# Kernel optimization log

Measured on AMD Instinct MI355X. Metric: run time of the kernel, lower is better.

## Reference

```python
import jax, jax.numpy as jnp
import numpy as np

EPS = 1e-5

def rms_norm(x, scale, eps=EPS):
    rms = jax.lax.rsqrt(jnp.mean(x * x, axis=-1, keepdims=True) + eps)
    return scale * (x * rms)

def act_quant(x, min_scale=0.001, max_scale=1000.0):
    # int8 activation quantization (STE in torch; fwd math only here)
    max_val = jnp.max(jnp.abs(x), axis=-1, keepdims=True)
    s = jnp.clip(127.0 / (max_val + 1e-5), min_scale, max_scale)
    return jnp.clip(jnp.round(s * x), -128.0, 127.0) / s

def weight_quant(w, num_bits=8):
    qmax = 2.0 ** (num_bits - 1) - 1.0
    scale = qmax / (jnp.max(jnp.abs(w)) + 1e-5)
    return jnp.round(jnp.clip(w * scale, -(qmax + 1.0), qmax)) / scale

def ternarize(w):
    sf = jnp.clip(1.0 / (jnp.mean(jnp.abs(w)) + 1e-5), 1e-4, 1e4)
    return jnp.sign(w * sf)

def setup_inputs() -> dict:
    key = jax.random.key(0)
    ks = jax.random.split(key, 5)
    B, S, E, H = 8, 512, 2048, 2048
    x = jax.random.normal(ks[0], (B, S, E), dtype=jnp.float32)
    # ternary {-1,0,1} init as in ternary_initialize
    def tern_init(k, shape):
        r = jax.random.uniform(k, shape, dtype=jnp.float32)
        return jnp.where(r < 1.0 / 3.0, -1.0, jnp.where(r > 2.0 / 3.0, 1.0, 0.0))
    return {
        "x": x,
        "rms_scale": jnp.ones((H,), jnp.float32),
        "W_f": tern_init(ks[1], (E, H)),
        "W_c": tern_init(ks[2], (E, H)),
        "W_g": tern_init(ks[3], (H, E)),
        "b_f": jnp.ones((H,), jnp.float32),
        "b_c": jnp.zeros((H,), jnp.float32),
        "b_g": jnp.zeros((H,), jnp.float32),
    }

def reference(x, rms_scale, W_f, W_c, W_g, b_f, b_c, b_g):
    B, S, E = x.shape
    H = W_f.shape[1]
    # quantize + ternarize weights once (identical every timestep)
    Wt_f = ternarize(weight_quant(W_f))
    Wt_c = ternarize(weight_quant(W_c))
    Wt_g = ternarize(weight_quant(W_g))  # (H, E) but E == H

    def step(h, x_t):
        xq = act_quant(rms_norm(x_t, rms_scale))
        # matmul-free linear: x @ (pos_mask - neg_mask) == x @ sign(W)
        f_t = jax.nn.sigmoid(xq @ Wt_f + b_f)
        c_t = jax.nn.silu(xq @ Wt_c + b_c)
        g_t = jax.nn.sigmoid(xq @ Wt_g + b_g)
        h_new = f_t * h + (1.0 - f_t) * c_t
        o_t = g_t * h_new
        # layer-level copy gate: sigmoid(W_g @ x_t^T)^T = sigmoid(x_t @ W_g^T), raw weights
        cg = jax.nn.sigmoid(x_t @ W_g.T)
        h_out = cg * x_t + (1.0 - cg) * h_new
        return h_out, o_t

    h0 = jnp.zeros((B, H), x.dtype)
    _, outs = jax.lax.scan(step, h0, jnp.swapaxes(x, 0, 1))  # scan over S
    return jnp.swapaxes(outs, 0, 1)  # (B, S, H)
```

## Files before the change

### kernel.cpp

```cpp
#include <hip/hip_runtime.h>
#include <hip/hip_bf16.h>
#include <cstdint>
#include <cstddef>

#define RTOT 4096
#define DIM  2048
#define NCAT 6144
#define NCHUNK 32
#define TCHUNK 16
#define NT 32

typedef __attribute__((ext_vector_type(4))) int int4v;

__device__ __forceinline__ float fast_sigmoid(float z) {
    return __builtin_amdgcn_rcpf(1.0f + __expf(-z));
}
__device__ __forceinline__ unsigned short f2h(float f) {
    union { _Float16 h; unsigned short u; } v; v.h = (_Float16)f; return v.u;
}
__device__ __forceinline__ float h2f(unsigned short u) {
    union { _Float16 h; unsigned short u; } v; v.u = u; return (float)v.h;
}

#define GLDS(gp, lp) __builtin_amdgcn_global_load_lds( \
    (__attribute__((address_space(1))) const void*)(gp), \
    (__attribute__((address_space(3))) void*)(lp), 16, 0, 0)

__device__ __forceinline__ int4v frag_ld(const signed char* p, int R, int lq) {
    return *(const int4v*)(p + R * 64 + ((lq ^ ((R >> 1) & 3)) * 16));
}

__global__ __launch_bounds__(256) void prep_all(
    const float* __restrict__ x, const float* __restrict__ scale,
    const float* __restrict__ Wf, const float* __restrict__ Wc,
    const float* __restrict__ Wg,
    signed char* __restrict__ WcatT, signed char* __restrict__ Wgb,
    signed char* __restrict__ Xq, signed char* __restrict__ Q1,
    signed char* __restrict__ Q2, float* __restrict__ s_arr,
    float* __restrict__ s1_arr)
{
    __shared__ __align__(16) char smem[4224];
    int bid = blockIdx.x;
    int tid = threadIdx.x;
    if (bid < 3072) {
        signed char (*tile)[65] = (signed char(*)[65])smem;
        int j0 = (bid % 96) * 64;
        int k0 = (bid / 96) * 64;
        const float* W = (j0 < 2048) ? Wf : (j0 < 4096) ? Wc : Wg;
        int jb = j0 & 2047;
        int c  = tid & 63;
        int rr = tid >> 6;
#pragma unroll
        for (int p = 0; p < 16; ++p) {
            int kl = p * 4 + rr;
            tile[kl][c] = (signed char)(int)W[(size_t)(k0 + kl) * DIM + jb + c];
        }
        __syncthreads();
#pragma unroll
        for (int p = 0; p < 16; ++p) {
            int jl = p * 4 + rr;
            WcatT[(size_t)(j0 + jl) * DIM + k0 + c] = tile[c][jl];
        }
    } else if (bid < 4096) {
        int idx = (bid - 3072) * 4096 + tid * 16;
#pragma unroll
        for (int p = 0; p < 4; ++p) {
            float4 v = *(const float4*)(Wg + idx + p * 4);
            char4 o;
            o.x = (signed char)(int)v.x; o.y = (signed char)(int)v.y;
            o.z = (signed char)(int)v.z; o.w = (signed char)(int)v.w;
            *(char4*)(Wgb + idx + p * 4) = o;
        }
    } else {
        int row = (bid - 4096) * 4 + (tid >> 6);
        int lane = tid & 63;
        const float* xr = x + (size_t)row * DIM;
        float xs[32], ys[32];
        float sum = 0.f, mx2 = 0.f;
#pragma unroll
        for (int sw = 0; sw < 4; ++sw) {
            int base = sw * 512 + lane * 8;
            float4 a0 = *(const float4*)(xr + base);
            float4 a1 = *(const float4*)(xr + base + 4);
            xs[sw * 8 + 0] = a0.x; xs[sw * 8 + 1] = a0.y;
            xs[sw * 8 + 2] = a0.z; xs[sw * 8 + 3] = a0.w;
            xs[sw * 8 + 4] = a1.x; xs[sw * 8 + 5] = a1.y;
            xs[sw * 8 + 6] = a1.z; xs[sw * 8 + 7] = a1.w;
        }
#pragma unroll
        for (int i = 0; i < 32; ++i) {
            sum += xs[i] * xs[i];
            mx2 = fmaxf(mx2, fabsf(xs[i]));
        }
#pragma unroll
        for (int off = 1; off < 64; off <<= 1) {
            sum += __shfl_xor(sum, off);
            mx2 = fmaxf(mx2, __shfl_xor(mx2, off));
        }
        float rms = 1.0f / sqrtf(sum * (1.0f / 2048.0f) + 1e-5f);
        float mx = 0.f;
#pragma unroll
        for (int sw = 0; sw < 4; ++sw) {
            int base = sw * 512 + lane * 8;
            float4 c0 = *(const float4*)(scale + base);
            float4 c1 = *(const float4*)(scale + base + 4);
            float scv[8] = {c0.x, c0.y, c0.z, c0.w, c1.x, c1.y, c1.z, c1.w};
#pragma unroll
            for (int i = 0; i < 8; ++i) {
                float yv = (xs[sw * 8 + i] * rms) * scv[i];
                ys[sw * 8 + i] = yv;
                mx = fmaxf(mx, fabsf(yv));
            }
        }
#pragma unroll
        for (int off = 1; off < 64; off <<= 1) mx = fmaxf(mx, __shfl_xor(mx, off));
        float s = 127.0f / (mx + 1e-5f);
        s = fminf(fmaxf(s, 0.001f), 1000.0f);
        float s1 = 127.0f / (mx2 + 1e-5f);
        float inv_s1 = 1.0f / s1;
        if (lane == 0) { s_arr[row] = s; s1_arr[row] = s1; }
#pragma unroll
        for (int sw = 0; sw < 4; ++sw) {
            signed char q8[8], q1b[8], q2b[8];
#pragma unroll
            for (int i = 0; i < 8; ++i) {
                float xv = xs[sw * 8 + i];
                float q = fminf(fmaxf(rintf(s * ys[sw * 8 + i]), -128.f), 127.f);
                q8[i] = (signed char)(int)q;
                float qq1 = fminf(fmaxf(rintf(s1 * xv), -128.f), 127.f);
                q1b[i] = (signed char)(int)qq1;
                float r = xv - qq1 * inv_s1;
                float qq2 = fminf(fmaxf(rintf(s1 * 256.f * r), -128.f), 127.f);
                q2b[i] = (signed char)(int)qq2;
            }
            size_t o = (size_t)row * DIM + sw * 512 + lane * 8;
            *(int2*)(Xq + o) = *(int2*)q8;
            *(int2*)(Q1 + o) = *(int2*)q1b;
            *(int2*)(Q2 + o) = *(int2*)q2b;
        }
    }
}

__global__ __launch_bounds__(512, 2) void gemm_all(
    const signed char* __restrict__ Xq, const signed char* __restrict__ WcatT,
    const signed char* __restrict__ Q1, const signed char* __restrict__ Q2,
    const signed char* __restrict__ Wgb,
    const float* __restrict__ s_arr, const float* __restrict__ s1_arr,
    const float* __restrict__ b_f, const float* __restrict__ b_c,
    const float* __restrict__ b_g,
    unsigned short* __restrict__ FCG,
    unsigned short* __restrict__ U,
    unsigned short* __restrict__ V)
{
    extern __shared__ __align__(16) signed char lds[];
    int bid = blockIdx.x;
    int grp = bid / 5, r5 = bid % 5;
    int tid = threadIdx.x;
    int lane = tid & 63, wv = tid >> 6;
    int lr = lane & 15, lq = lane >> 4;
    int srow = wv * 16 + (lane >> 2);
    int ssw  = ((lane & 3) ^ ((srow >> 1) & 3)) * 16;
    const size_t ustep = (size_t)128 * DIM;

    if (r5 < 3) {
        int fb = grp * 3 + r5;
        int m0 = (fb & 15) * 256;
        int n0 = (fb >> 4) * 256;
        int wm = (wv >> 2) * 128;
        int wn = (wv & 3) * 64;
        const signed char* Ab = Xq + (size_t)m0 * DIM;
        const signed char* Bb = WcatT + (size_t)n0 * DIM;
        const signed char* gA = Ab + (size_t)srow * DIM + ssw;
        const signed char* gB = Bb + (size_t)srow * DIM + ssw;

        int4v acc[8][4] = {};
        int4v a[4], b[4];

#pragma unroll
        for (int t0 = 0; t0 < 2; ++t0) {
            signed char* sb = lds + t0 * 32768;
            GLDS(gA + t0 * 64,         sb + wv * 1024);
            GLDS(gA + ustep + t0 * 64, sb + 8192 + wv * 1024);
            GLDS(gB + t0 * 64,         sb + 16384 + wv * 1024);
            GLDS(gB + ustep + t0 * 64, sb + 16384 + 8192 + wv * 1024);
        }

        int bc = 0, bn = 1, bs = 2;
        for (int t = 0; t < NT; ++t) {
            if (t == NT - 1) { asm volatile("s_waitcnt vmcnt(0)" ::: "memory"); }
            else             { asm volatile("s_waitcnt vmcnt(4)" ::: "memory"); }
            __builtin_amdgcn_sched_barrier(0);
            __builtin_amdgcn_s_barrier();
            __builtin_amdgcn_sched_barrier(0);
            const signed char* cA = lds + bc * 32768;
            const signed char* cB = cA + 16384;
            signed char* sA = lds + bs * 32768;
            signed char* sB = sA + 16384;
            int kt2 = (t + 2) * 64;
            bool st = (t + 2 < NT);

#pragma unroll
            for (int i = 0; i < 4; ++i) a[i] = frag_ld(cA, wm + i * 16 + lr, lq);
#pragma unroll
            for (int j = 0; j < 4; ++j) b[j] = frag_ld(cB, wn + j * 16 + lr, lq);
            if (st) {
                GLDS(gA + kt2,         sA + wv * 1024);
                GLDS(gA + ustep + kt2, sA + 8192 + wv * 1024);
            }
            __builtin_amdgcn_s_barrier();
            asm volatile("s_waitcnt lgkmcnt(0)" ::: "memory");
            __builtin_amdgcn_sched_barrier(0);
            __builtin_amdgcn_s_setprio(1);
#pragma unroll
            for (int i = 0; i < 4; ++i)
#pragma unroll
                for (int j = 0; j < 4; ++j)
                    acc[i][j] = __builtin_amdgcn_mfma_i32_16x16x64_i8(
                        a[i], b[j], acc[i][j], 0, 0, 0);
            __builtin_amdgcn_s_setprio(0);
            __builtin_amdgcn_s_barrier();

#pragma unroll
            for (int i = 0; i < 4; ++i) a[i] = frag_ld(cA, wm + (4 + i) * 16 + lr, lq);
            if (st) {
                GLDS(gB + kt2,         sB + wv * 1024);
                GLDS(gB + ustep + kt2, sB + 8192 + wv * 1024);
            }
            __builtin_amdgcn_s_barrier();
            asm volatile("s_waitcnt lgkmcnt(0)" ::: "memory");
            __builtin_amdgcn_sched_barrier(0);
            __builtin_amdgcn_s_setprio(1);
#pragma unroll
            for (int i = 0; i < 4; ++i)
#pragma unroll
                for (int j = 0; j < 4; ++j)
                    acc[4 + i][j] = __builtin_amdgcn_mfma_i32_16x16x64_i8(
                        a[i], b[j], acc[4 + i][j], 0, 0, 0);
            __builtin_amdgcn_s_setprio(0);
            __builtin_amdgcn_s_barrier();

            int tmp = bc; bc = bn; bn = bs; bs = tmp;
        }

        int rowb = m0 + wm;
#pragma unroll
        for (int mi = 0; mi < 8; ++mi) {
            float rinv[4];
#pragma unroll
            for (int r = 0; r < 4; ++r)
                rinv[r] = __builtin_amdgcn_rcpf(s_arr[rowb + mi * 16 + lq * 4 + r]);
#pragma unroll
            for (int ni = 0; ni < 4; ++ni) {
                int gcol = n0 + wn + ni * 16 + lr;
                int sec = gcol >> 11;
                int jj = gcol & 2047;
                float bias = (sec == 0) ? b_f[jj] : (sec == 1) ? b_c[jj] : b_g[jj];
#pragma unroll
                for (int r = 0; r < 4; ++r) {
                    int grow = rowb + mi * 16 + lq * 4 + r;
                    float z = fmaf((float)acc[mi][ni][r], rinv[r], bias);
                    float sg = fast_sigmoid(z);
                    FCG[(size_t)grow * NCAT + gcol] = f2h((sec == 1) ? z * sg : sg);
                }
            }
        }
    } else {
        int cb = grp * 2 + (r5 - 3);
        int m0 = (cb & 15) * 256;
        int n0 = (cb >> 4) * 128;
        int wm = (wv >> 2) * 128;
        int wn = (wv & 3) * 32;
        const signed char* A1b = Q1 + (size_t)m0 * DIM;
        const signed char* A2b = Q2 + (size_t)m0 * DIM;
        const signed char* Bb  = Wgb + (size_t)n0 * DIM;
        const signed char* g1 = A1b + (size_t)srow * DIM + ssw;
        const signed char* g2 = A2b + (size_t)srow * DIM + ssw;
        const signed char* gB = Bb + (size_t)srow * DIM + ssw;

        int4v acc1[8][2] = {};
        int4v acc2[8][2] = {};
        int4v a1[8], a2[8], b[2];

#pragma unroll
        for (int t0 = 0; t0 < 2; ++t0) {
            signed char* sb = lds + t0 * 40960;
            GLDS(g1 + t0 * 64,         sb + wv * 1024);
            GLDS(g1 + ustep + t0 * 64, sb + 8192 + wv * 1024);
            GLDS(gB + t0 * 64,         sb + 32768 + wv * 1024);
            GLDS(g2 + t0 * 64,         sb + 16384 + wv * 1024);
            GLDS(g2 + ustep + t0 * 64, sb + 16384 + 8192 + wv * 1024);
        }

        int bc = 0, bn = 1, bs = 2;
        for (int t = 0; t < NT; ++t) {
            if (t == NT - 1) { asm volatile("s_waitcnt vmcnt(0)" ::: "memory"); }
            else             { asm volatile("s_waitcnt vmcnt(5)" ::: "memory"); }
            __builtin_amdgcn_sched_barrier(0);
            __builtin_amdgcn_s_barrier();
            __builtin_amdgcn_sched_barrier(0);
            const signed char* cA1 = lds + bc * 40960;
            const signed char* cA2 = cA1 + 16384;
            const signed char* cB  = cA1 + 32768;
            signed char* s1p = lds + bs * 40960;
            signed char* s2p = s1p + 16384;
            signed char* sBp = s1p + 32768;
            int kt2 = (t + 2) * 64;
            bool st = (t + 2 < NT);

#pragma unroll
            for (int i = 0; i < 8; ++i) a1[i] = frag_ld(cA1, wm + i * 16 + lr, lq);
#pragma unroll
            for (int j = 0; j < 2; ++j) b[j] = frag_ld(cB, wn + j * 16 + lr, lq);
            if (st) {
                GLDS(g1 + kt2,         s1p + wv * 1024);
                GLDS(g1 + ustep + kt2, s1p + 8192 + wv * 1024);
                GLDS(gB + kt2,         sBp + wv * 1024);
            }
            __builtin_amdgcn_s_barrier();
            asm volatile("s_waitcnt lgkmcnt(0)" ::: "memory");
            __builtin_amdgcn_sched_barrier(0);
            __builtin_amdgcn_s_setprio(1);
#pragma unroll
            for (int i = 0; i < 8; ++i)
#pragma unroll
                for (int j = 0; j < 2; ++j)
                    acc1[i][j] = __builtin_amdgcn_mfma_i32_16x16x64_i8(
                        a1[i], b[j], acc1[i][j], 0, 0, 0);
            __builtin_amdgcn_s_setprio(0);
            __builtin_amdgcn_s_barrier();

#pragma unroll
            for (int i = 0; i < 8; ++i) a2[i] = frag_ld(cA2, wm + i * 16 + lr, lq);
            if (st) {
                GLDS(g2 + kt2,         s2p + wv * 1024);
                GLDS(g2 + ustep + kt2, s2p + 8192 + wv * 1024);
            }
            __builtin_amdgcn_s_barrier();
            asm volatile("s_waitcnt lgkmcnt(0)" ::: "memory");
            __builtin_amdgcn_sched_barrier(0);
            __builtin_amdgcn_s_setprio(1);
#pragma unroll
            for (int i = 0; i < 8; ++i)
#pragma unroll
                for (int j = 0; j < 2; ++j)
                    acc2[i][j] = __builtin_amdgcn_mfma_i32_16x16x64_i8(
                        a2[i], b[j], acc2[i][j], 0, 0, 0);
            __builtin_amdgcn_s_setprio(0);
            __builtin_amdgcn_s_barrier();

            int tmp = bc; bc = bn; bn = bs; bs = tmp;
        }

        int rowb = m0 + wm;
#pragma unroll
        for (int mi = 0; mi < 8; ++mi) {
            float rinv[4];
#pragma unroll
            for (int r = 0; r < 4; ++r)
                rinv[r] = __builtin_amdgcn_rcpf(s1_arr[rowb + mi * 16 + lq * 4 + r]);
#pragma unroll
            for (int ni = 0; ni < 2; ++ni) {
                int gcol = n0 + wn + ni * 16 + lr;
#pragma unroll
                for (int r = 0; r < 4; ++r) {
                    int grow = rowb + mi * 16 + lq * 4 + r;
                    size_t go = (size_t)grow * DIM + gcol;
                    float zs = (float)acc1[mi][ni][r] + (float)acc2[mi][ni][r] * (1.f / 256.f);
                    float cg = fast_sigmoid(zs * rinv[r]);
                    float xv = ((float)Q1[go] + (float)Q2[go] * (1.f / 256.f)) * rinv[r];
                    U[go] = f2h(cg * xv);
                    V[go] = f2h(1.f - cg);
                }
            }
        }
    }
}

__global__ __launch_bounds__(256) void scan_partial(
    const unsigned short* __restrict__ FCG, const unsigned short* __restrict__ U,
    const unsigned short* __restrict__ V, float4* __restrict__ PQ4)
{
    int tp = blockIdx.x * 256 + threadIdx.x;
    int c = blockIdx.y;
    int b = blockIdx.z;
    int h0 = tp * 2;
    size_t r0 = (size_t)(b * 512 + c * TCHUNK);
    const unsigned short* fp = FCG + r0 * NCAT + h0;
    const unsigned short* up = U + r0 * DIM + h0;
    const unsigned short* vp = V + r0 * DIM + h0;
    float P0 = 1.f, Q0 = 0.f, P1 = 1.f, Q1v = 0.f;
#pragma unroll 4
    for (int t = 0; t < TCHUNK; ++t) {
        unsigned fw = *(const unsigned*)(fp);
        unsigned cw = *(const unsigned*)(fp + 2048);
        unsigned uw = *(const unsigned*)(up);
        unsigned vw = *(const unsigned*)(vp);
        float f0 = h2f(fw & 0xffff), f1 = h2f(fw >> 16);
        float c0 = h2f(cw & 0xffff), c1 = h2f(cw >> 16);
        float u0 = h2f(uw & 0xffff), u1 = h2f(uw >> 16);
        float v0 = h2f(vw & 0xffff), v1 = h2f(vw >> 16);
        float A0 = v0 * f0, A1 = v1 * f1;
        float B0 = fmaf(v0 * (1.f - f0), c0, u0);
        float B1 = fmaf(v1 * (1.f - f1), c1, u1);
        P0 = A0 * P0; Q0 = fmaf(A0, Q0, B0);
        P1 = A1 * P1; Q1v = fmaf(A1, Q1v, B1);
        fp += NCAT; up += DIM; vp += DIM;
    }
    float4 o; o.x = P0; o.y = Q0; o.z = P1; o.w = Q1v;
    PQ4[(size_t)c * 8192 + b * 1024 + tp] = o;
}

__global__ __launch_bounds__(256) void scan_final(
    const unsigned short* __restrict__ FCG, const unsigned short* __restrict__ U,
    const unsigned short* __restrict__ V, const float4* __restrict__ PQ4,
    float* __restrict__ out)
{
    int tp = blockIdx.x * 256 + threadIdx.x;
    int c = blockIdx.y;
    int b = blockIdx.z;
    int h0 = tp * 2;
    float h0s = 0.f, h1s = 0.f;
#pragma unroll 4
    for (int cc = 0; cc < c; ++cc) {
        float4 pq = PQ4[(size_t)cc * 8192 + b * 1024 + tp];
        h0s = fmaf(pq.x, h0s, pq.y);
        h1s = fmaf(pq.z, h1s, pq.w);
    }
    size_t r0 = (size_t)(b * 512 + c * TCHUNK);
    const unsigned short* fp = FCG + r0 * NCAT + h0;
    const unsigned short* up = U + r0 * DIM + h0;
    const unsigned short* vp = V + r0 * DIM + h0;
    float* op = out + r0 * DIM + h0;
#pragma unroll 4
    for (int t = 0; t < TCHUNK; ++t) {
        unsigned fw = *(const unsigned*)(fp);
        unsigned cw = *(const unsigned*)(fp + 2048);
        unsigned gw = *(const unsigned*)(fp + 4096);
        unsigned uw = *(const unsigned*)(up);
        unsigned vw = *(const unsigned*)(vp);
        float f0 = h2f(fw & 0xffff), f1 = h2f(fw >> 16);
        float c0 = h2f(cw & 0xffff), c1 = h2f(cw >> 16);
        float g0 = h2f(gw & 0xffff), g1 = h2f(gw >> 16);
        float u0 = h2f(uw & 0xffff), u1 = h2f(uw >> 16);
        float v0 = h2f(vw & 0xffff), v1 = h2f(vw >> 16);
        float hn0 = f0 * h0s + (1.f - f0) * c0;
        float hn1 = f1 * h1s + (1.f - f1) * c1;
        float2 ov; ov.x = g0 * hn0; ov.y = g1 * hn1;
        *(float2*)op = ov;
        h0s = fmaf(v0, hn0, u0);
        h1s = fmaf(v1, hn1, u1);
        fp += NCAT; up += DIM; vp += DIM; op += DIM;
    }
}

extern "C" void kernel_launch(void* const* d_in, const int* in_sizes, int n_in,
                              void* d_out, int out_size, void* d_ws, size_t ws_size,
                              hipStream_t stream) {
    const float* x     = (const float*)d_in[0];
    const float* rmssc = (const float*)d_in[1];
    const float* W_f   = (const float*)d_in[2];
    const float* W_c   = (const float*)d_in[3];
    const float* W_g   = (const float*)d_in[4];
    const float* b_f   = (const float*)d_in[5];
    const float* b_c   = (const float*)d_in[6];
    const float* b_g   = (const float*)d_in[7];
    float* out = (float*)d_out;

    char* ws = (char*)d_ws;
    size_t off = 0;
    auto alloc = [&](size_t bytes) -> void* {
        void* p = ws + off;
        off += (bytes + 255) & ~(size_t)255;
        return p;
    };
    signed char* WcatT = (signed char*)alloc((size_t)NCAT * DIM);
    signed char* Wgb   = (signed char*)alloc((size_t)DIM * DIM);
    signed char* Xq    = (signed char*)alloc((size_t)RTOT * DIM);
    signed char* Q1    = (signed char*)alloc((size_t)RTOT * DIM);
    signed char* Q2    = (signed char*)alloc((size_t)RTOT * DIM);
    float* s_arr       = (float*)alloc((size_t)RTOT * 4);
    float* s1_arr      = (float*)alloc((size_t)RTOT * 4);
    unsigned short* FCG = (unsigned short*)alloc((size_t)RTOT * NCAT * 2);
    unsigned short* U   = (unsigned short*)alloc((size_t)RTOT * DIM * 2);
    unsigned short* V   = (unsigned short*)alloc((size_t)RTOT * DIM * 2);
    float4* PQ4        = (float4*)alloc((size_t)NCHUNK * 8192 * 16);

    static int gemm_attr_once = [](){
        return (int)hipFuncSetAttribute((const void*)gemm_all,
                   hipFuncAttributeMaxDynamicSharedMemorySize, 3 * 40960);
    }();
    (void)gemm_attr_once;

    hipLaunchKernelGGL(prep_all, dim3(5120), dim3(256), 0, stream,
                       x, rmssc, W_f, W_c, W_g, WcatT, Wgb, Xq, Q1, Q2,
                       s_arr, s1_arr);
    hipLaunchKernelGGL(gemm_all, dim3(640), dim3(512), 3 * 40960, stream,
                       Xq, WcatT, Q1, Q2, Wgb, s_arr, s1_arr,
                       b_f, b_c, b_g, FCG, U, V);
    hipLaunchKernelGGL(scan_partial, dim3(DIM / 512, NCHUNK - 1, 8), dim3(256), 0, stream,
                       FCG, U, V, PQ4);
    hipLaunchKernelGGL(scan_final, dim3(DIM / 512, NCHUNK, 8), dim3(256), 0, stream,
                       FCG, U, V, PQ4, out);
}
```

Baseline: 275.3 us.

## Shrink GEMM tiles to 128x128 with 256-thread blocks and double buffering

Rewrites the fused int8 GEMM kernel to use 128x128 (and 128x64 for the copy-gate path) tiles, 256-thread blocks and 2-stage LDS double buffering in place of 256x256 tiles, 512 threads and a 3-stage pipeline. The grid grows from 640 to 2560 blocks. The aim is more blocks, better occupancy and less LDS per block, which should balance load across CUs and simplify the barrier schedule. In exchange, operands are reused less per tile and the shallower prefetch, with a full vmcnt(0) wait every iteration, can expose global-load latency.

```diff
diff --git a/kernel.cpp b/kernel.cpp
--- a/kernel.cpp
+++ b/kernel.cpp
@@ -141,7 +141,7 @@
     }
 }
 
-__global__ __launch_bounds__(512, 2) void gemm_all(
+__global__ __launch_bounds__(256, 3) void gemm_all(
     const signed char* __restrict__ Xq, const signed char* __restrict__ WcatT,
     const signed char* __restrict__ Q1, const signed char* __restrict__ Q2,
     const signed char* __restrict__ Wgb,
@@ -160,54 +160,42 @@
     int lr = lane & 15, lq = lane >> 4;
     int srow = wv * 16 + (lane >> 2);
     int ssw  = ((lane & 3) ^ ((srow >> 1) & 3)) * 16;
-    const size_t ustep = (size_t)128 * DIM;
+    const size_t ustep = (size_t)64 * DIM;
 
     if (r5 < 3) {
         int fb = grp * 3 + r5;
-        int m0 = (fb & 15) * 256;
-        int n0 = (fb >> 4) * 256;
-        int wm = (wv >> 2) * 128;
-        int wn = (wv & 3) * 64;
-        const signed char* Ab = Xq + (size_t)m0 * DIM;
-        const signed char* Bb = WcatT + (size_t)n0 * DIM;
-        const signed char* gA = Ab + (size_t)srow * DIM + ssw;
-        const signed char* gB = Bb + (size_t)srow * DIM + ssw;
-
-        int4v acc[8][4] = {};
+        int m0 = (fb & 31) * 128;
+        int n0 = (fb >> 5) * 128;
+        int wm = (wv >> 1) * 64, wn = (wv & 1) * 64;
+        const signed char* gA = Xq + (size_t)(m0 + srow) * DIM + ssw;
+        const signed char* gB = WcatT + (size_t)(n0 + srow) * DIM + ssw;
+
+        int4v acc[4][4] = {};
         int4v a[4], b[4];
 
-#pragma unroll
-        for (int t0 = 0; t0 < 2; ++t0) {
-            signed char* sb = lds + t0 * 32768;
-            GLDS(gA + t0 * 64,         sb + wv * 1024);
-            GLDS(gA + ustep + t0 * 64, sb + 8192 + wv * 1024);
-            GLDS(gB + t0 * 64,         sb + 16384 + wv * 1024);
-            GLDS(gB + ustep + t0 * 64, sb + 16384 + 8192 + wv * 1024);
-        }
-
-        int bc = 0, bn = 1, bs = 2;
+        GLDS(gA,         lds + wv * 1024);
+        GLDS(gA + ustep, lds + 4096 + wv * 1024);
+        GLDS(gB,         lds + 8192 + wv * 1024);
+        GLDS(gB + ustep, lds + 12288 + wv * 1024);
+
         for (int t = 0; t < NT; ++t) {
-            if (t == NT - 1) { asm volatile("s_waitcnt vmcnt(0)" ::: "memory"); }
-            else             { asm volatile("s_waitcnt vmcnt(4)" ::: "memory"); }
+            asm volatile("s_waitcnt vmcnt(0)" ::: "memory");
             __builtin_amdgcn_sched_barrier(0);
             __builtin_amdgcn_s_barrier();
             __builtin_amdgcn_sched_barrier(0);
-            const signed char* cA = lds + bc * 32768;
-            const signed char* cB = cA + 16384;
-            signed char* sA = lds + bs * 32768;
-            signed char* sB = sA + 16384;
-            int kt2 = (t + 2) * 64;
-            bool st = (t + 2 < NT);
-
-#pragma unroll
-            for (int i = 0; i < 4; ++i) a[i] = frag_ld(cA, wm + i * 16 + lr, lq);
-#pragma unroll
-            for (int j = 0; j < 4; ++j) b[j] = frag_ld(cB, wn + j * 16 + lr, lq);
-            if (st) {
-                GLDS(gA + kt2,         sA + wv * 1024);
-                GLDS(gA + ustep + kt2, sA + 8192 + wv * 1024);
-            }
-            __builtin_amdgcn_s_barrier();
+            const signed char* cur = lds + (t & 1) * 16384;
+            signed char* nxt = lds + ((t + 1) & 1) * 16384;
+#pragma unroll
+            for (int i = 0; i < 4; ++i) a[i] = frag_ld(cur, wm + i * 16 + lr, lq);
+#pragma unroll
+            for (int j = 0; j < 4; ++j) b[j] = frag_ld(cur + 8192, wn + j * 16 + lr, lq);
+            if (t + 1 < NT) {
+                int kt = (t + 1) * 64;
+                GLDS(gA + kt,         nxt + wv * 1024);
+                GLDS(gA + ustep + kt, nxt + 4096 + wv * 1024);
+                GLDS(gB + kt,         nxt + 8192 + wv * 1024);
+                GLDS(gB + ustep + kt, nxt + 12288 + wv * 1024);
+            }
             asm volatile("s_waitcnt lgkmcnt(0)" ::: "memory");
             __builtin_amdgcn_sched_barrier(0);
             __builtin_amdgcn_s_setprio(1);
@@ -218,33 +206,11 @@
                     acc[i][j] = __builtin_amdgcn_mfma_i32_16x16x64_i8(
                         a[i], b[j], acc[i][j], 0, 0, 0);
             __builtin_amdgcn_s_setprio(0);
-            __builtin_amdgcn_s_barrier();
-
-#pragma unroll
-            for (int i = 0; i < 4; ++i) a[i] = frag_ld(cA, wm + (4 + i) * 16 + lr, lq);
-            if (st) {
-                GLDS(gB + kt2,         sB + wv * 1024);
-                GLDS(gB + ustep + kt2, sB + 8192 + wv * 1024);
-            }
-            __builtin_amdgcn_s_barrier();
-            asm volatile("s_waitcnt lgkmcnt(0)" ::: "memory");
-            __builtin_amdgcn_sched_barrier(0);
-            __builtin_amdgcn_s_setprio(1);
-#pragma unroll
-            for (int i = 0; i < 4; ++i)
-#pragma unroll
-                for (int j = 0; j < 4; ++j)
-                    acc[4 + i][j] = __builtin_amdgcn_mfma_i32_16x16x64_i8(
-                        a[i], b[j], acc[4 + i][j], 0, 0, 0);
-            __builtin_amdgcn_s_setprio(0);
-            __builtin_amdgcn_s_barrier();
-
-            int tmp = bc; bc = bn; bn = bs; bs = tmp;
         }
 
         int rowb = m0 + wm;
 #pragma unroll
-        for (int mi = 0; mi < 8; ++mi) {
+        for (int mi = 0; mi < 4; ++mi) {
             float rinv[4];
 #pragma unroll
             for (int r = 0; r < 4; ++r)
@@ -266,94 +232,63 @@
         }
     } else {
         int cb = grp * 2 + (r5 - 3);
-        int m0 = (cb & 15) * 256;
-        int n0 = (cb >> 4) * 128;
-        int wm = (wv >> 2) * 128;
-        int wn = (wv & 3) * 32;
-        const signed char* A1b = Q1 + (size_t)m0 * DIM;
-        const signed char* A2b = Q2 + (size_t)m0 * DIM;
-        const signed char* Bb  = Wgb + (size_t)n0 * DIM;
-        const signed char* g1 = A1b + (size_t)srow * DIM + ssw;
-        const signed char* g2 = A2b + (size_t)srow * DIM + ssw;
-        const signed char* gB = Bb + (size_t)srow * DIM + ssw;
-
-        int4v acc1[8][2] = {};
-        int4v acc2[8][2] = {};
-        int4v a1[8], a2[8], b[2];
-
-#pragma unroll
-        for (int t0 = 0; t0 < 2; ++t0) {
-            signed char* sb = lds + t0 * 40960;
-            GLDS(g1 + t0 * 64,         sb + wv * 1024);
-            GLDS(g1 + ustep + t0 * 64, sb + 8192 + wv * 1024);
-            GLDS(gB + t0 * 64,         sb + 32768 + wv * 1024);
-            GLDS(g2 + t0 * 64,         sb + 16384 + wv * 1024);
-            GLDS(g2 + ustep + t0 * 64, sb + 16384 + 8192 + wv * 1024);
-        }
-
-        int bc = 0, bn = 1, bs = 2;
+        int m0 = (cb & 31) * 128;
+        int n0 = (cb >> 5) * 64;
+        int wm = (wv >> 1) * 64, wn = (wv & 1) * 32;
+        const signed char* g1 = Q1 + (size_t)(m0 + srow) * DIM + ssw;
+        const signed char* g2 = Q2 + (size_t)(m0 + srow) * DIM + ssw;
+        const signed char* gB = Wgb + (size_t)(n0 + srow) * DIM + ssw;
+
+        int4v acc1[4][2] = {};
+        int4v acc2[4][2] = {};
+        int4v a1[4], a2[4], b[2];
+
+        GLDS(g1,         lds + wv * 1024);
+        GLDS(g1 + ustep, lds + 4096 + wv * 1024);
+        GLDS(g2,         lds + 8192 + wv * 1024);
+        GLDS(g2 + ustep, lds + 12288 + wv * 1024);
+        GLDS(gB,         lds + 16384 + wv * 1024);
+
         for (int t = 0; t < NT; ++t) {
-            if (t == NT - 1) { asm volatile("s_waitcnt vmcnt(0)" ::: "memory"); }
-            else             { asm volatile("s_waitcnt vmcnt(5)" ::: "memory"); }
+            asm volatile("s_waitcnt vmcnt(0)" ::: "memory");
             __builtin_amdgcn_sched_barrier(0);
             __builtin_amdgcn_s_barrier();
             __builtin_amdgcn_sched_barrier(0);
-            const signed char* cA1 = lds + bc * 40960;
-            const signed char* cA2 = cA1 + 16384;
-            const signed char* cB  = cA1 + 32768;
-            signed char* s1p = lds + bs * 40960;
-            signed char* s2p = s1p + 16384;
-            signed char* sBp = s1p + 32768;
-            int kt2 = (t + 2) * 64;
-            bool st = (t + 2 < NT);
-
-#pragma unroll
-            for (int i = 0; i < 8; ++i) a1[i] = frag_ld(cA1, wm + i * 16 + lr, lq);
-#pragma unroll
-            for (int j = 0; j < 2; ++j) b[j] = frag_ld(cB, wn + j * 16 + lr, lq);
-            if (st) {
-                GLDS(g1 + kt2,         s1p + wv * 1024);
-                GLDS(g1 + ustep + kt2, s1p + 8192 + wv * 1024);
-                GLDS(gB + kt2,         sBp + wv * 1024);
-            }
-            __builtin_amdgcn_s_barrier();
+            const signed char* cur = lds + (t & 1) * 20480;
+            signed char* nxt = lds + ((t + 1) & 1) * 20480;
+#pragma unroll
+            for (int i = 0; i < 4; ++i) {
+                a1[i] = frag_ld(cur, wm + i * 16 + lr, lq);
+                a2[i] = frag_ld(cur + 8192, wm + i * 16 + lr, lq);
+            }
+#pragma unroll
+            for (int j = 0; j < 2; ++j) b[j] = frag_ld(cur + 16384, wn + j * 16 + lr, lq);
+            if (t + 1 < NT) {
+                int kt = (t + 1) * 64;
+                GLDS(g1 + kt,         nxt + wv * 1024);
+                GLDS(g1 + ustep + kt, nxt + 4096 + wv * 1024);
+                GLDS(g2 + kt,         nxt + 8192 + wv * 1024);
+                GLDS(g2 + ustep + kt, nxt + 12288 + wv * 1024);
+                GLDS(gB + kt,         nxt + 16384 + wv * 1024);
+            }
             asm volatile("s_waitcnt lgkmcnt(0)" ::: "memory");
             __builtin_amdgcn_sched_barrier(0);
             __builtin_amdgcn_s_setprio(1);
 #pragma unroll
-            for (int i = 0; i < 8; ++i)
-#pragma unroll
-                for (int j = 0; j < 2; ++j)
+            for (int i = 0; i < 4; ++i)
+#pragma unroll
+                for (int j = 0; j < 2; ++j) {
                     acc1[i][j] = __builtin_amdgcn_mfma_i32_16x16x64_i8(
                         a1[i], b[j], acc1[i][j], 0, 0, 0);
-            __builtin_amdgcn_s_setprio(0);
-            __builtin_amdgcn_s_barrier();
-
-#pragma unroll
-            for (int i = 0; i < 8; ++i) a2[i] = frag_ld(cA2, wm + i * 16 + lr, lq);
-            if (st) {
-                GLDS(g2 + kt2,         s2p + wv * 1024);
-                GLDS(g2 + ustep + kt2, s2p + 8192 + wv * 1024);
-            }
-            __builtin_amdgcn_s_barrier();
-            asm volatile("s_waitcnt lgkmcnt(0)" ::: "memory");
-            __builtin_amdgcn_sched_barrier(0);
-            __builtin_amdgcn_s_setprio(1);
-#pragma unroll
-            for (int i = 0; i < 8; ++i)
-#pragma unroll
-                for (int j = 0; j < 2; ++j)
                     acc2[i][j] = __builtin_amdgcn_mfma_i32_16x16x64_i8(
                         a2[i], b[j], acc2[i][j], 0, 0, 0);
+                }
             __builtin_amdgcn_s_setprio(0);
-            __builtin_amdgcn_s_barrier();
-
-            int tmp = bc; bc = bn; bn = bs; bs = tmp;
         }
 
         int rowb = m0 + wm;
 #pragma unroll
-        for (int mi = 0; mi < 8; ++mi) {
+        for (int mi = 0; mi < 4; ++mi) {
             float rinv[4];
 #pragma unroll
             for (int r = 0; r < 4; ++r)
@@ -485,16 +420,10 @@
     unsigned short* V   = (unsigned short*)alloc((size_t)RTOT * DIM * 2);
     float4* PQ4        = (float4*)alloc((size_t)NCHUNK * 8192 * 16);
 
-    static int gemm_attr_once = [](){
-        return (int)hipFuncSetAttribute((const void*)gemm_all,
-                   hipFuncAttributeMaxDynamicSharedMemorySize, 3 * 40960);
-    }();
-    (void)gemm_attr_once;
-
     hipLaunchKernelGGL(prep_all, dim3(5120), dim3(256), 0, stream,
                        x, rmssc, W_f, W_c, W_g, WcatT, Wgb, Xq, Q1, Q2,
                        s_arr, s1_arr);
-    hipLaunchKernelGGL(gemm_all, dim3(640), dim3(512), 3 * 40960, stream,
+    hipLaunchKernelGGL(gemm_all, dim3(2560), dim3(256), 49152, stream,
                        Xq, WcatT, Q1, Q2, Wgb, s_arr, s1_arr,
                        b_f, b_c, b_g, FCG, U, V);
     hipLaunchKernelGGL(scan_partial, dim3(DIM / 512, NCHUNK - 1, 8), dim3(256), 0, stream,
```

Measured after the change: 288.1 us. +4.6%, slower.
